# Performance work log

Measured on AMD Instinct MI355X. Metric: run time of the kernel, lower is better.

## Reference

```python
import jax, jax.numpy as jnp
import numpy as np

B, N, D, V, K = 64, 256, 512, 50257, 100
NORM_TERM = float(np.log(V))        # norm_term='auto' -> log(vocab)
BACKOFF_PROB = 1e-10


def setup_inputs() -> dict:
    key = jax.random.key(0)
    k1, k2, k3, k4, k5 = jax.random.split(key, 5)
    inp = jax.random.normal(k1, (B, N, D), jnp.float32)
    emb_weight = jax.random.normal(k2, (V, D), jnp.float32) * 0.02
    emb_bias = jnp.zeros((V,), jnp.float32)
    # noise distribution buffer: probs clamped + renormed, then log (as in __init__)
    freqs = jax.random.uniform(k3, (V,), jnp.float32, 1e-3, 1.0)
    probs = freqs / freqs.sum()
    probs = jnp.clip(probs, BACKOFF_PROB)
    logprob_noise = jnp.log(probs / probs.sum())
    target = jax.random.randint(k4, (B, N), 0, V)
    # alias.draw(1,1,K).expand(B,N,K): a single shared set of K noise samples
    noise_samples = jax.random.randint(k5, (K,), 0, V)
    return {
        "input": inp,
        "emb_weight": emb_weight,
        "emb_bias": emb_bias,
        "logprob_noise": logprob_noise,
        "target": target,
        "noise_samples": noise_samples,
    }


def reference(input, emb_weight, emb_bias, logprob_noise, target, noise_samples):
    k = noise_samples.shape[0]
    # logits under the noise distribution (pure gathers)
    logit_target_in_noise = logprob_noise[target]          # (B, N)
    logit_noise_in_noise = logprob_noise[noise_samples]    # (K,)
    # model scores: gathered embedding rows dotted with hidden states
    tgt_emb = emb_weight[target]                           # (B, N, D)
    logit_target_in_model = (
        jnp.einsum("bnd,bnd->bn", input, tgt_emb) + emb_bias[target] - NORM_TERM
    )                                                      # (B, N)
    noise_emb = emb_weight[noise_samples]                  # (K, D)
    logit_noise_in_model = (
        jnp.einsum("bnd,kd->bnk", input, noise_emb)
        + emb_bias[noise_samples][None, None, :]
        - NORM_TERM
    )                                                      # (B, N, K)
    # NCE: p_true = exp(lm) / (exp(lm) + K*exp(ln)) = sigmoid(lm - ln - log K)
    # BCE with label [1, 0, ..., 0]:
    #   -loss = log_sigmoid(x) at target slot, log_sigmoid(-x) at noise slots
    log_k = jnp.log(jnp.asarray(k, dtype=input.dtype))
    x_t = logit_target_in_model - logit_target_in_noise - log_k             # (B, N)
    x_n = logit_noise_in_model - logit_noise_in_noise[None, None, :] - log_k  # (B, N, K)
    per_pos = jax.nn.log_sigmoid(x_t) + jnp.sum(jax.nn.log_sigmoid(-x_n), axis=2)
    return jnp.sum(per_pos, axis=1)  # (B,)
```

## Files before the change

### kernel.cpp

```cpp
#include <hip/hip_runtime.h>
#include <math.h>

#define Dq 512
#define Vq 50257
#define Kq 100
#define KP 112
#define NORM_TERM 10.8249051f
#define LOGK 4.6051702f
#define NBLK 512
#define DT_STRIDE 3584

typedef __attribute__((ext_vector_type(8))) short short8;
typedef __attribute__((ext_vector_type(4))) float floatx4;
typedef __attribute__((ext_vector_type(4))) unsigned short ushort4v;
typedef __attribute__((ext_vector_type(8))) unsigned short ushort8v;

__device__ __forceinline__ unsigned short f2bf(float f) {
    union { float f; unsigned u; } v; v.f = f;
    unsigned r = v.u + 0x7FFFu + ((v.u >> 16) & 1u);
    return (unsigned short)(r >> 16);
}

__device__ __forceinline__ short8 cvt8(floatx4 a, floatx4 b) {
    short8 o;
    o[0] = (short)f2bf(a.x); o[1] = (short)f2bf(a.y);
    o[2] = (short)f2bf(a.z); o[3] = (short)f2bf(a.w);
    o[4] = (short)f2bf(b.x); o[5] = (short)f2bf(b.y);
    o[6] = (short)f2bf(b.z); o[7] = (short)f2bf(b.w);
    return o;
}

__device__ __forceinline__ float dot4(floatx4 a, floatx4 b) {
    return a.x*b.x + a.y*b.y + a.z*b.z + a.w*b.w;
}

__device__ __forceinline__ float log_sigmoid(float x) {
    return fminf(x, 0.f) - __logf(1.f + __expf(-fabsf(x)));
}

__global__ void prep_noise(const float* __restrict__ emb_w,
                           const float* __restrict__ emb_b,
                           const float* __restrict__ lpn,
                           const int* __restrict__ ns,
                           unsigned short* __restrict__ nBT,
                           float* __restrict__ nAdj) {
    int k = blockIdx.x;
    int t = threadIdx.x;
    size_t off = (size_t)(t >> 3) * DT_STRIDE + k * 32 + (t & 7) * 4;
    if (k < Kq) {
        int row = ns[k];
        floatx4 v = ((const floatx4*)(emb_w + (size_t)row * Dq))[t];
        ushort4v o;
        o.x = f2bf(v.x); o.y = f2bf(v.y); o.z = f2bf(v.z); o.w = f2bf(v.w);
        *(ushort4v*)(nBT + off) = o;
        if (t == 0) nAdj[k] = emb_b[row] - NORM_TERM - lpn[row] - LOGK;
    } else {
        ushort4v z; z.x = 0; z.y = 0; z.z = 0; z.w = 0;
        *(ushort4v*)(nBT + off) = z;
        if (t == 0) nAdj[k] = 0.f;
    }
}

__global__ __launch_bounds__(512, 4) void nce_main(
    const float* __restrict__ input,
    const float* __restrict__ emb_w,
    const float* __restrict__ emb_b,
    const float* __restrict__ lpn,
    const int* __restrict__ target,
    const unsigned short* __restrict__ nBT,
    const float* __restrict__ nAdj,
    float* __restrict__ partials)
{
    __shared__ unsigned short A_lds[32 * 512];
    __shared__ float tdot[32];

    int tid  = threadIdx.x;
    int lane = tid & 63;
    int w    = tid >> 6;
    int pos0 = (int)blockIdx.x * 32;
    int r16  = lane & 15;
    int g4   = lane >> 4;

#pragma unroll
    for (int j = 0; j < 4; ++j) {
        int row = w * 4 + j;
        const float* src = input + (size_t)(pos0 + row) * Dq + lane * 8;
        int tg = target[pos0 + row];
        const float* tsrc = emb_w + (size_t)tg * Dq + lane * 8;
        floatx4 x0 = *(const floatx4*)(src);
        floatx4 x1 = *(const floatx4*)(src + 4);
        floatx4 t0 = *(const floatx4*)(tsrc);
        floatx4 t1 = *(const floatx4*)(tsrc + 4);
        float s = dot4(x0, t0) + dot4(x1, t1);
#pragma unroll
        for (int off = 32; off >= 1; off >>= 1)
            s += __shfl_xor(s, off);
        if (lane == 0) tdot[row] = s;
        char* base = (char*)A_lds + row * 1024;
        *(ushort8v*)(base + ((lane * 16) ^ ((row & 7) << 4))) = (ushort8v)cvt8(x0, x1);
    }
    __syncthreads();

    float contrib = 0.f;

    if (w < 7) {
        const char* a0base = (const char*)A_lds + r16 * 1024;
        const char* a1base = a0base + 16 * 1024;
        int asw = (r16 & 7) << 4;
        const unsigned short* p = nBT + (size_t)w * 512 + r16 * 32 + g4 * 8;
        floatx4 acc0 = {0.f, 0.f, 0.f, 0.f};
        floatx4 acc1 = {0.f, 0.f, 0.f, 0.f};
#pragma unroll
        for (int dt = 0; dt < 16; ++dt) {
            int aoff = (dt * 64 + g4 * 16) ^ asw;
            short8 a0 = *(const short8*)(a0base + aoff);
            short8 a1 = *(const short8*)(a1base + aoff);
            short8 f  = *(const short8*)(p + (size_t)dt * DT_STRIDE);
            acc0 = __builtin_amdgcn_mfma_f32_16x16x32_bf16(a0, f, acc0, 0, 0, 0);
            acc1 = __builtin_amdgcn_mfma_f32_16x16x32_bf16(a1, f, acc1, 0, 0, 0);
        }
        int k = w * 16 + r16;
        if (k < Kq) {
            float adj = nAdj[k];
#pragma unroll
            for (int r = 0; r < 4; ++r) {
                contrib += log_sigmoid(-(acc0[r] + adj));
                contrib += log_sigmoid(-(acc1[r] + adj));
            }
        }
    } else {
        if (g4 < 2) {
            int p32 = g4 * 16 + r16;
            int tg = target[pos0 + p32];
            float xt = tdot[p32] + emb_b[tg] - NORM_TERM - lpn[tg] - LOGK;
            contrib += log_sigmoid(xt);
        }
    }

#pragma unroll
    for (int off = 32; off >= 1; off >>= 1)
        contrib += __shfl_xor(contrib, off);
    if (lane == 0) partials[(size_t)blockIdx.x * 8 + w] = contrib;
}

__global__ void finalize(const float* __restrict__ partials,
                         float* __restrict__ out) {
    __shared__ float s4[64][5];
    int t = threadIdx.x;
    int b = t >> 2, q = t & 3;
    float s = 0.f;
#pragma unroll
    for (int i = 0; i < 16; ++i) s += partials[b * 64 + q * 16 + i];
    s4[b][q] = s;
    __syncthreads();
    if (t < 64) out[t] = s4[t][0] + s4[t][1] + s4[t][2] + s4[t][3];
}

extern "C" void kernel_launch(void* const* d_in, const int* in_sizes, int n_in,
                              void* d_out, int out_size, void* d_ws, size_t ws_size,
                              hipStream_t stream) {
    const float* input = (const float*)d_in[0];
    const float* emb_w = (const float*)d_in[1];
    const float* emb_b = (const float*)d_in[2];
    const float* lpn   = (const float*)d_in[3];
    const int*   tgt   = (const int*)d_in[4];
    const int*   ns    = (const int*)d_in[5];
    float* out = (float*)d_out;

    unsigned short* nBT = (unsigned short*)d_ws;
    float* nAdj     = (float*)((char*)d_ws + (size_t)KP * Dq * 2);
    float* partials = (float*)((char*)d_ws + (size_t)KP * Dq * 2 + 512);

    prep_noise<<<KP, 128, 0, stream>>>(emb_w, emb_b, lpn, ns, nBT, nAdj);
    nce_main<<<NBLK, 512, 0, stream>>>(input, emb_w, emb_b, lpn, tgt, nBT, nAdj,
                                       partials);
    finalize<<<1, 256, 0, stream>>>(partials, out);
}
```

Before: 27.28 us.

## Pre-convert input to bf16 tiled layout in prep, drop LDS staging and finalize kernel

Moves the fp32-to-bf16 conversion of the hidden states into the prep kernel, which writes them in an MFMA-friendly tiled global layout. The main kernel then reads A fragments straight from global memory, with no shared-memory staging and no __syncthreads. The finalize kernel is replaced by per-block atomicAdd into the output, which prep zeroes first. The cost is an extra full pass over the input: it is read in fp32 for conversion, written back as bf16, and read again in the main kernel (which also still reads fp32 input for the target dot). Float atomics also make the summation order nondeterministic.

```diff
diff --git a/kernel.cpp b/kernel.cpp
--- a/kernel.cpp
+++ b/kernel.cpp
@@ -9,25 +9,16 @@
 #define LOGK 4.6051702f
 #define NBLK 512
 #define DT_STRIDE 3584
+#define PSP (16416 * 32)
 
 typedef __attribute__((ext_vector_type(8))) short short8;
 typedef __attribute__((ext_vector_type(4))) float floatx4;
 typedef __attribute__((ext_vector_type(4))) unsigned short ushort4v;
-typedef __attribute__((ext_vector_type(8))) unsigned short ushort8v;
 
 __device__ __forceinline__ unsigned short f2bf(float f) {
     union { float f; unsigned u; } v; v.f = f;
     unsigned r = v.u + 0x7FFFu + ((v.u >> 16) & 1u);
     return (unsigned short)(r >> 16);
-}
-
-__device__ __forceinline__ short8 cvt8(floatx4 a, floatx4 b) {
-    short8 o;
-    o[0] = (short)f2bf(a.x); o[1] = (short)f2bf(a.y);
-    o[2] = (short)f2bf(a.z); o[3] = (short)f2bf(a.w);
-    o[4] = (short)f2bf(b.x); o[5] = (short)f2bf(b.y);
-    o[6] = (short)f2bf(b.z); o[7] = (short)f2bf(b.w);
-    return o;
 }
 
 __device__ __forceinline__ float dot4(floatx4 a, floatx4 b) {
@@ -38,26 +29,43 @@
     return fminf(x, 0.f) - __logf(1.f + __expf(-fabsf(x)));
 }
 
-__global__ void prep_noise(const float* __restrict__ emb_w,
-                           const float* __restrict__ emb_b,
-                           const float* __restrict__ lpn,
-                           const int* __restrict__ ns,
-                           unsigned short* __restrict__ nBT,
-                           float* __restrict__ nAdj) {
-    int k = blockIdx.x;
-    int t = threadIdx.x;
-    size_t off = (size_t)(t >> 3) * DT_STRIDE + k * 32 + (t & 7) * 4;
-    if (k < Kq) {
-        int row = ns[k];
-        floatx4 v = ((const floatx4*)(emb_w + (size_t)row * Dq))[t];
-        ushort4v o;
-        o.x = f2bf(v.x); o.y = f2bf(v.y); o.z = f2bf(v.z); o.w = f2bf(v.w);
-        *(ushort4v*)(nBT + off) = o;
-        if (t == 0) nAdj[k] = emb_b[row] - NORM_TERM - lpn[row] - LOGK;
+__global__ void prep(const float* __restrict__ emb_w,
+                     const float* __restrict__ emb_b,
+                     const float* __restrict__ lpn,
+                     const int* __restrict__ ns,
+                     const float* __restrict__ input,
+                     unsigned short* __restrict__ nBT,
+                     float* __restrict__ nAdj,
+                     unsigned short* __restrict__ inT,
+                     float* __restrict__ out) {
+    int bid = blockIdx.x;
+    int t   = threadIdx.x;
+    if (bid < KP) {
+        int k = bid;
+        size_t off = (size_t)(t >> 3) * DT_STRIDE + k * 32 + (t & 7) * 4;
+        if (k < Kq) {
+            int row = ns[k];
+            floatx4 v = ((const floatx4*)(emb_w + (size_t)row * Dq))[t];
+            ushort4v o;
+            o.x = f2bf(v.x); o.y = f2bf(v.y); o.z = f2bf(v.z); o.w = f2bf(v.w);
+            *(ushort4v*)(nBT + off) = o;
+            if (t == 0) nAdj[k] = emb_b[row] - NORM_TERM - lpn[row] - LOGK;
+        } else {
+            ushort4v z; z.x = 0; z.y = 0; z.z = 0; z.w = 0;
+            *(ushort4v*)(nBT + off) = z;
+            if (t == 0) nAdj[k] = 0.f;
+        }
+        if (bid == 0 && t < 64) out[t] = 0.f;
     } else {
-        ushort4v z; z.x = 0; z.y = 0; z.z = 0; z.w = 0;
-        *(ushort4v*)(nBT + off) = z;
-        if (t == 0) nAdj[k] = 0.f;
+        int r0 = (bid - KP) * 8;
+#pragma unroll
+        for (int j = 0; j < 8; ++j) {
+            int row = r0 + j;
+            floatx4 v = ((const floatx4*)(input + (size_t)row * Dq))[t];
+            ushort4v o;
+            o.x = f2bf(v.x); o.y = f2bf(v.y); o.z = f2bf(v.z); o.w = f2bf(v.w);
+            *(ushort4v*)(inT + (size_t)(t >> 3) * PSP + (size_t)row * 32 + (t & 7) * 4) = o;
+        }
     }
 }
 
@@ -69,11 +77,9 @@
     const int* __restrict__ target,
     const unsigned short* __restrict__ nBT,
     const float* __restrict__ nAdj,
-    float* __restrict__ partials)
+    const unsigned short* __restrict__ inT,
+    float* __restrict__ out)
 {
-    __shared__ unsigned short A_lds[32 * 512];
-    __shared__ float tdot[32];
-
     int tid  = threadIdx.x;
     int lane = tid & 63;
     int w    = tid >> 6;
@@ -81,12 +87,14 @@
     int r16  = lane & 15;
     int g4   = lane >> 4;
 
+    float contrib = 0.f;
+
 #pragma unroll
     for (int j = 0; j < 4; ++j) {
-        int row = w * 4 + j;
-        const float* src = input + (size_t)(pos0 + row) * Dq + lane * 8;
-        int tg = target[pos0 + row];
-        const float* tsrc = emb_w + (size_t)tg * Dq + lane * 8;
+        int pos = pos0 + 4 * w + j;
+        int tg  = target[pos];
+        const float* src  = input + (size_t)pos * Dq + lane * 8;
+        const float* tsrc = emb_w + (size_t)tg  * Dq + lane * 8;
         floatx4 x0 = *(const floatx4*)(src);
         floatx4 x1 = *(const floatx4*)(src + 4);
         floatx4 t0 = *(const floatx4*)(tsrc);
@@ -95,29 +103,22 @@
 #pragma unroll
         for (int off = 32; off >= 1; off >>= 1)
             s += __shfl_xor(s, off);
-        if (lane == 0) tdot[row] = s;
-        char* base = (char*)A_lds + row * 1024;
-        *(ushort8v*)(base + ((lane * 16) ^ ((row & 7) << 4))) = (ushort8v)cvt8(x0, x1);
+        if (lane == 0)
+            contrib += log_sigmoid(s + emb_b[tg] - NORM_TERM - lpn[tg] - LOGK);
     }
-    __syncthreads();
-
-    float contrib = 0.f;
 
     if (w < 7) {
-        const char* a0base = (const char*)A_lds + r16 * 1024;
-        const char* a1base = a0base + 16 * 1024;
-        int asw = (r16 & 7) << 4;
-        const unsigned short* p = nBT + (size_t)w * 512 + r16 * 32 + g4 * 8;
+        const unsigned short* pa = inT + (size_t)(pos0 + r16) * 32 + g4 * 8;
+        const unsigned short* pb = nBT + (size_t)w * 512 + r16 * 32 + g4 * 8;
         floatx4 acc0 = {0.f, 0.f, 0.f, 0.f};
         floatx4 acc1 = {0.f, 0.f, 0.f, 0.f};
 #pragma unroll
         for (int dt = 0; dt < 16; ++dt) {
-            int aoff = (dt * 64 + g4 * 16) ^ asw;
-            short8 a0 = *(const short8*)(a0base + aoff);
-            short8 a1 = *(const short8*)(a1base + aoff);
-            short8 f  = *(const short8*)(p + (size_t)dt * DT_STRIDE);
-            acc0 = __builtin_amdgcn_mfma_f32_16x16x32_bf16(a0, f, acc0, 0, 0, 0);
-            acc1 = __builtin_amdgcn_mfma_f32_16x16x32_bf16(a1, f, acc1, 0, 0, 0);
+            short8 a0 = *(const short8*)(pa + (size_t)dt * PSP);
+            short8 a1 = *(const short8*)(pa + (size_t)dt * PSP + 16 * 32);
+            short8 b  = *(const short8*)(pb + (size_t)dt * DT_STRIDE);
+            acc0 = __builtin_amdgcn_mfma_f32_16x16x32_bf16(a0, b, acc0, 0, 0, 0);
+            acc1 = __builtin_amdgcn_mfma_f32_16x16x32_bf16(a1, b, acc1, 0, 0, 0);
         }
         int k = w * 16 + r16;
         if (k < Kq) {
@@ -128,32 +129,13 @@
                 contrib += log_sigmoid(-(acc1[r] + adj));
             }
         }
-    } else {
-        if (g4 < 2) {
-            int p32 = g4 * 16 + r16;
-            int tg = target[pos0 + p32];
-            float xt = tdot[p32] + emb_b[tg] - NORM_TERM - lpn[tg] - LOGK;
-            contrib += log_sigmoid(xt);
-        }
     }
 
 #pragma unroll
     for (int off = 32; off >= 1; off >>= 1)
         contrib += __shfl_xor(contrib, off);
-    if (lane == 0) partials[(size_t)blockIdx.x * 8 + w] = contrib;
-}
-
-__global__ void finalize(const float* __restrict__ partials,
-                         float* __restrict__ out) {
-    __shared__ float s4[64][5];
-    int t = threadIdx.x;
-    int b = t >> 2, q = t & 3;
-    float s = 0.f;
-#pragma unroll
-    for (int i = 0; i < 16; ++i) s += partials[b * 64 + q * 16 + i];
-    s4[b][q] = s;
-    __syncthreads();
-    if (t < 64) out[t] = s4[t][0] + s4[t][1] + s4[t][2] + s4[t][3];
+    if (lane == 0)
+        atomicAdd(&out[blockIdx.x >> 3], contrib);
 }
 
 extern "C" void kernel_launch(void* const* d_in, const int* in_sizes, int n_in,
@@ -168,11 +150,11 @@
     float* out = (float*)d_out;
 
     unsigned short* nBT = (unsigned short*)d_ws;
-    float* nAdj     = (float*)((char*)d_ws + (size_t)KP * Dq * 2);
-    float* partials = (float*)((char*)d_ws + (size_t)KP * Dq * 2 + 512);
+    float* nAdj         = (float*)((char*)d_ws + (size_t)KP * Dq * 2);
+    unsigned short* inT = (unsigned short*)((char*)d_ws + (size_t)KP * Dq * 2 + 512);
 
-    prep_noise<<<KP, 128, 0, stream>>>(emb_w, emb_b, lpn, ns, nBT, nAdj);
-    nce_main<<<NBLK, 512, 0, stream>>>(input, emb_w, emb_b, lpn, tgt, nBT, nAdj,
-                                       partials);
-    finalize<<<1, 256, 0, stream>>>(partials, out);
+    prep<<<KP + 2048, 128, 0, stream>>>(emb_w, emb_b, lpn, ns, input,
+                                        nBT, nAdj, inT, out);
+    nce_main<<<NBLK, 512, 0, stream>>>(input, emb_w, emb_b, lpn, tgt,
+                                       nBT, nAdj, inT, out);
 }
```

Result: slower. 57.51 us (+110.9%).
